# Kernel optimization log

Hardware: AMD Instinct MI355X
Metric: run time of the kernel (lower is better)

Reference implementation:

```python
import jax, jax.numpy as jnp
import numpy as np

# ---- static config ----
H, W = 60, 60
WS = 7          # window size (square)
SS = 3          # shift size
DIM = 256
NH = 8
HD = DIM // NH
N = WS * WS     # tokens per window = 49
HP = (H // WS + 1) * WS  # 63 (padded, matches __init__ mask construction)
WP = (W // WS + 1) * WS  # 63
NW = (HP // WS) * (WP // WS)  # 81 windows
EPS = 1e-5


def _rel_pos_index():
    coords = np.stack(np.meshgrid(np.arange(WS), np.arange(WS), indexing='ij'))  # (2,WS,WS)
    cf = coords.reshape(2, -1)                      # (2, N)
    rel = cf[:, :, None] - cf[:, None, :]           # (2, N, N)
    rel = rel.transpose(1, 2, 0).astype(np.int64)   # (N, N, 2)
    rel[..., 0] += WS - 1
    rel[..., 1] += WS - 1
    rel[..., 0] *= 2 * WS - 1
    return rel.sum(-1)                              # (N, N) in [0, 169)


def _attn_mask():
    img = np.zeros((HP, WP), dtype=np.float32)
    cnt = 0
    for hs in (slice(0, -WS), slice(-WS, -SS), slice(-SS, None)):
        for ws_ in (slice(0, -WS), slice(-WS, -SS), slice(-SS, None)):
            img[hs, ws_] = cnt
            cnt += 1
    mw = img.reshape(HP // WS, WS, WP // WS, WS).transpose(0, 2, 1, 3).reshape(-1, N)  # (NW, N)
    diff = mw[:, None, :] - mw[:, :, None]          # (NW, N, N)
    return np.where(diff != 0, -100.0, 0.0).astype(np.float32)


REL_IDX = _rel_pos_index()
ATTN_MASK = _attn_mask()


def layer_norm(x, g, b):
    mu = jnp.mean(x, axis=-1, keepdims=True)
    var = jnp.mean(jnp.square(x - mu), axis=-1, keepdims=True)
    return (x - mu) * jax.lax.rsqrt(var + EPS) * g + b


def setup_inputs() -> dict:
    key = jax.random.key(0)
    ks = jax.random.split(key, 8)
    B = 24
    std = 0.02
    return {
        'x': jax.random.normal(ks[0], (B, H * W, DIM), jnp.float32),
        'g1': jnp.ones((DIM,), jnp.float32),
        'b1': jnp.zeros((DIM,), jnp.float32),
        'w_qkv': jax.random.normal(ks[1], (DIM, 3 * DIM), jnp.float32) * std,
        'b_qkv': jnp.zeros((3 * DIM,), jnp.float32),
        'rel_bias_table': jax.random.normal(ks[2], ((2 * WS - 1) ** 2, NH), jnp.float32) * std,
        'w_proj': jax.random.normal(ks[3], (DIM, DIM), jnp.float32) * std,
        'b_proj': jnp.zeros((DIM,), jnp.float32),
        'g2': jnp.ones((DIM,), jnp.float32),
        'b2': jnp.zeros((DIM,), jnp.float32),
        'w_fc1': jax.random.normal(ks[4], (DIM, 4 * DIM), jnp.float32) * std,
        'b_fc1': jnp.zeros((4 * DIM,), jnp.float32),
        'w_fc2': jax.random.normal(ks[5], (4 * DIM, DIM), jnp.float32) * std,
        'b_fc2': jnp.zeros((DIM,), jnp.float32),
    }


def _swin_block(x, g1, b1, w_qkv, b_qkv, rel_bias_table, w_proj, b_proj,
                g2, b2, w_fc1, b_fc1, w_fc2, b_fc2):
    B, L, C = x.shape
    shortcut = x
    x = layer_norm(x, g1, b1).reshape(B, H, W, C)
    # pad to (HP, WP)
    x = jnp.pad(x, ((0, 0), (0, HP - H), (0, WP - W), (0, 0)))
    # cyclic shift
    x = jnp.roll(x, (-SS, -SS), axis=(1, 2))
    # window partition -> (B*NW, N, C)
    xw = x.reshape(B, HP // WS, WS, WP // WS, WS, C).transpose(0, 1, 3, 2, 4, 5)
    xw = xw.reshape(B * NW, N, C)
    # attention
    qkv = (xw @ w_qkv + b_qkv).reshape(B * NW, N, 3, NH, HD).transpose(2, 0, 3, 1, 4)
    q, k, v = qkv[0], qkv[1], qkv[2]            # (B*NW, NH, N, HD)
    q = q * (HD ** -0.5)
    attn = jnp.einsum('whnd,whmd->whnm', q, k)  # (B*NW, NH, N, N)
    rel_bias = rel_bias_table[jnp.asarray(REL_IDX)]          # (N, N, NH)
    attn = attn + rel_bias.transpose(2, 0, 1)[None]
    mask = jnp.asarray(ATTN_MASK)                            # (NW, N, N)
    attn = attn.reshape(B, NW, NH, N, N) + mask[None, :, None]
    attn = jax.nn.softmax(attn.reshape(B * NW, NH, N, N), axis=-1)
    out = jnp.einsum('whnm,whmd->whnd', attn, v)             # (B*NW, NH, N, HD)
    out = out.transpose(0, 2, 1, 3).reshape(B * NW, N, C)
    out = out @ w_proj + b_proj
    # window reverse -> (B, HP, WP, C)
    out = out.reshape(B, HP // WS, WP // WS, WS, WS, C).transpose(0, 1, 3, 2, 4, 5)
    out = out.reshape(B, HP, WP, C)
    # reverse shift, unpad
    out = jnp.roll(out, (SS, SS), axis=(1, 2))[:, :H, :W, :].reshape(B, L, C)
    x = shortcut + out
    # MLP
    y = layer_norm(x, g2, b2)
    y = jax.nn.gelu(y @ w_fc1 + b_fc1, approximate=False) @ w_fc2 + b_fc2
    return x + y


def reference(x, g1, b1, w_qkv, b_qkv, rel_bias_table, w_proj, b_proj,
              g2, b2, w_fc1, b_fc1, w_fc2, b_fc2):
    return _swin_block(x, g1, b1, w_qkv, b_qkv, rel_bias_table, w_proj, b_proj,
                       g2, b2, w_fc1, b_fc1, w_fc2, b_fc2)
```

## Files before the change

kernel.cpp:

```cpp
#include <hip/hip_runtime.h>
#include <hip/hip_bf16.h>
#include <math.h>


typedef _Float16 half8 __attribute__((ext_vector_type(8)));
typedef _Float16 half4_t __attribute__((ext_vector_type(4)));
typedef float f32x4 __attribute__((ext_vector_type(4)));

#define GLDS16(gp, lp)                                                    \
  __builtin_amdgcn_global_load_lds(                                      \
      (__attribute__((address_space(1))) const void*)(gp),               \
      (__attribute__((address_space(3))) void*)(lp), 16, 0, 0)

__device__ __forceinline__ float wave_reduce_sum(float v) {
  v += __shfl_xor(v, 1);
  v += __shfl_xor(v, 2);
  v += __shfl_xor(v, 4);
  v += __shfl_xor(v, 8);
  v += __shfl_xor(v, 16);
  v += __shfl_xor(v, 32);
  return v;
}

__global__ __launch_bounds__(256) void prep_weights(
    const float* __restrict__ wqkv, const float* __restrict__ wproj,
    const float* __restrict__ wfc1, const float* __restrict__ wfc2,
    _Float16* __restrict__ oqkv, _Float16* __restrict__ oproj,
    _Float16* __restrict__ ofc1, _Float16* __restrict__ ofc2)
{
  int idx = blockIdx.x * 256 + threadIdx.x;
  if (idx < 196608) {
    int n = idx / 256, k = idx % 256;
    oqkv[idx] = (_Float16)wqkv[k * 768 + n];
  } else if (idx < 262144) {
    int i = idx - 196608; int n = i / 256, k = i % 256;
    oproj[i] = (_Float16)wproj[k * 256 + n];
  } else if (idx < 524288) {
    int i = idx - 262144; int n = i / 256, k = i % 256;
    ofc1[i] = (_Float16)wfc1[k * 1024 + n];
  } else {
    int i = idx - 524288; int n = i / 1024, k = i % 1024;
    ofc2[i] = (_Float16)wfc2[k * 256 + n];
  }
}

__global__ __launch_bounds__(256) void prep_cb(
    const float* __restrict__ rbt, _Float16* __restrict__ cbt)
{
  int idx = blockIdx.x * 256 + threadIdx.x;
  int m = idx & 63, n = (idx >> 6) & 63;
  int hc = idx >> 12; int h = hc & 7, c = hc >> 3;
  float v;
  if (n < 49 && m < 49) {
    int i1 = n / 7, j1 = n % 7, i2 = m / 7, j2 = m % 7;
    float bias = rbt[((i1 - i2 + 6) * 13 + (j1 - j2 + 6)) * 8 + h];
    int rh1 = (c & 2) ? (i1 < 4 ? 1 : 2) : 0;
    int rh2 = (c & 2) ? (i2 < 4 ? 1 : 2) : 0;
    int rw1 = (c & 1) ? (j1 < 4 ? 1 : 2) : 0;
    int rw2 = (c & 1) ? (j2 < 4 ? 1 : 2) : 0;
    v = bias + (((rh1 != rh2) || (rw1 != rw2)) ? -100.f : 0.f);
  } else {
    v = -60000.f;
  }
  cbt[idx] = (_Float16)v;
}

__global__ __launch_bounds__(256) void ln1_window_kernel(
    const float* __restrict__ x, const float* __restrict__ g,
    const float* __restrict__ bta, _Float16* __restrict__ xw,
    int row0, int rows_c)
{
  int lrow = blockIdx.x * 4 + (threadIdx.x >> 6);
  if (lrow >= rows_c) return;
  int row = row0 + lrow;
  int lane = threadIdx.x & 63;
  int bw = row / 49, n = row - bw * 49;
  int b = bw / 81, win = bw - b * 81;
  int wh = win / 9, ww = win - wh * 9;
  int i = n / 7, j = n - i * 7;
  int sh = wh * 7 + i + 3; if (sh >= 63) sh -= 63;
  int sw = ww * 7 + j + 3; if (sw >= 63) sw -= 63;
  bool valid = (sh < 60) && (sw < 60);
  float4 v = make_float4(0.f, 0.f, 0.f, 0.f);
  if (valid)
    v = reinterpret_cast<const float4*>(x + ((size_t)b * 3600 + sh * 60 + sw) * 256)[lane];
  float s = v.x + v.y + v.z + v.w;
  s = wave_reduce_sum(s);
  float mu = s * (1.f / 256.f);
  float dx = v.x - mu, dy = v.y - mu, dz = v.z - mu, dw = v.w - mu;
  float q = dx * dx + dy * dy + dz * dz + dw * dw;
  q = wave_reduce_sum(q);
  float rs = rsqrtf(q * (1.f / 256.f) + 1e-5f);
  float4 gv = reinterpret_cast<const float4*>(g)[lane];
  float4 bv = reinterpret_cast<const float4*>(bta)[lane];
  union { _Float16 h[4]; uint2 u; } pk;
  if (valid) {
    pk.h[0] = (_Float16)(dx * rs * gv.x + bv.x);
    pk.h[1] = (_Float16)(dy * rs * gv.y + bv.y);
    pk.h[2] = (_Float16)(dz * rs * gv.z + bv.z);
    pk.h[3] = (_Float16)(dw * rs * gv.w + bv.w);
  } else {
    pk.h[0] = pk.h[1] = pk.h[2] = pk.h[3] = (_Float16)0.f;
  }
  *reinterpret_cast<uint2*>(xw + (size_t)lrow * 256 + lane * 4) = pk.u;
}

__global__ __launch_bounds__(256) void ln2_kernel(
    const float* __restrict__ xin, const float* __restrict__ g,
    const float* __restrict__ bta, _Float16* __restrict__ y)
{
  int row = blockIdx.x * 4 + (threadIdx.x >> 6);
  int lane = threadIdx.x & 63;
  float4 v = reinterpret_cast<const float4*>(xin + (size_t)row * 256)[lane];
  float s = v.x + v.y + v.z + v.w;
  s = wave_reduce_sum(s);
  float mu = s * (1.f / 256.f);
  float dx = v.x - mu, dy = v.y - mu, dz = v.z - mu, dw = v.w - mu;
  float q = dx * dx + dy * dy + dz * dz + dw * dw;
  q = wave_reduce_sum(q);
  float rs = rsqrtf(q * (1.f / 256.f) + 1e-5f);
  float4 gv = reinterpret_cast<const float4*>(g)[lane];
  float4 bv = reinterpret_cast<const float4*>(bta)[lane];
  union { _Float16 h[4]; uint2 u; } pk;
  pk.h[0] = (_Float16)(dx * rs * gv.x + bv.x);
  pk.h[1] = (_Float16)(dy * rs * gv.y + bv.y);
  pk.h[2] = (_Float16)(dz * rs * gv.z + bv.z);
  pk.h[3] = (_Float16)(dw * rs * gv.w + bv.w);
  *reinterpret_cast<uint2*>(y + (size_t)row * 256 + lane * 4) = pk.u;
}

__global__ __launch_bounds__(256) void gemm_kernel(
    const _Float16* __restrict__ A, const _Float16* __restrict__ Bt,
    const float* __restrict__ bias, const float* __restrict__ resid,
    void* __restrict__ out, int M, int N, int K, int mode, int row0)
{
  __shared__ __align__(16) _Float16 As[4096];
  __shared__ __align__(16) _Float16 Bs[4096];
  const int tid = threadIdx.x;
  const int m0 = blockIdx.x * 128, n0 = blockIdx.y * 128;
  const int wv = tid >> 6, ln = tid & 63;
  const int wm = (wv >> 1) * 64, wn = (wv & 1) * 64;
  const int quad = ln >> 4, l16 = ln & 15;

  const int r0 = wv * 32 + (ln >> 2);
  const int r1 = r0 + 16;
  const int sg0 = (((ln & 3) ^ ((r0 >> 1) & 3)) << 3);
  const int sg1 = (((ln & 3) ^ ((r1 >> 1) & 3)) << 3);
  int gmA0 = m0 + r0; if (gmA0 >= M) gmA0 = M - 1;
  int gmA1 = m0 + r1; if (gmA1 >= M) gmA1 = M - 1;
  const _Float16* pA0 = A + (size_t)gmA0 * K + sg0;
  const _Float16* pA1 = A + (size_t)gmA1 * K + sg1;
  const _Float16* pB0 = Bt + (size_t)(n0 + r0) * K + sg0;
  const _Float16* pB1 = Bt + (size_t)(n0 + r1) * K + sg1;
  _Float16* ldsA0 = As + wv * 1024;
  _Float16* ldsA1 = As + wv * 1024 + 512;
  _Float16* ldsB0 = Bs + wv * 1024;
  _Float16* ldsB1 = Bs + wv * 1024 + 512;

  const half8* pa[4]; const half8* pb[4];
#pragma unroll
  for (int i = 0; i < 4; i++) {
    int ra = wm + i * 16 + l16;
    pa[i] = reinterpret_cast<const half8*>(&As[ra * 32 + ((quad ^ ((ra >> 1) & 3)) << 3)]);
    int rb = wn + i * 16 + l16;
    pb[i] = reinterpret_cast<const half8*>(&Bs[rb * 32 + ((quad ^ ((rb >> 1) & 3)) << 3)]);
  }

  f32x4 acc[4][4];
#pragma unroll
  for (int i = 0; i < 4; i++)
#pragma unroll
    for (int j = 0; j < 4; j++) acc[i][j] = (f32x4)0.f;

  for (int k0 = 0; k0 < K; k0 += 32) {
    GLDS16(pA0 + k0, ldsA0);
    GLDS16(pA1 + k0, ldsA1);
    GLDS16(pB0 + k0, ldsB0);
    GLDS16(pB1 + k0, ldsB1);
    __syncthreads();
    half8 af[4], bf[4];
#pragma unroll
    for (int i = 0; i < 4; i++) { af[i] = *pa[i]; bf[i] = *pb[i]; }
#pragma unroll
    for (int i = 0; i < 4; i++)
#pragma unroll
      for (int j = 0; j < 4; j++)
        acc[i][j] = __builtin_amdgcn_mfma_f32_16x16x32_f16(af[i], bf[j], acc[i][j], 0, 0, 0);
    __syncthreads();
  }

  float bq[4];
#pragma unroll
  for (int j = 0; j < 4; j++) bq[j] = bias[n0 + wn + j * 16 + l16];

#pragma unroll
  for (int i = 0; i < 4; i++) {
#pragma unroll
    for (int r = 0; r < 4; r++) {
      int gm = m0 + wm + i * 16 + quad * 4 + r;
      if (gm >= M) continue;
      if (mode == 0) {
        _Float16* op = reinterpret_cast<_Float16*>(out) + (size_t)gm * N;
#pragma unroll
        for (int j = 0; j < 4; j++) {
          int gn = n0 + wn + j * 16 + l16;
          float v = acc[i][j][r] + bq[j];
          if (gn < 256) v *= 0.17677669529663687f;
          op[gn] = (_Float16)v;
        }
      } else if (mode == 2) {
        _Float16* op = reinterpret_cast<_Float16*>(out) + (size_t)gm * N;
#pragma unroll
        for (int j = 0; j < 4; j++) {
          int gn = n0 + wn + j * 16 + l16;
          float v = acc[i][j][r] + bq[j];
          v = 0.5f * v * (1.f + erff(v * 0.70710678118654752f));
          op[gn] = (_Float16)v;
        }
      } else if (mode == 3) {
        float* op = reinterpret_cast<float*>(out) + (size_t)gm * N;
        const float* rp = resid + (size_t)gm * N;
#pragma unroll
        for (int j = 0; j < 4; j++) {
          int gn = n0 + wn + j * 16 + l16;
          op[gn] = rp[gn] + acc[i][j][r] + bq[j];
        }
      } else {
        int gmg = gm + row0;
        int bw = gmg / 49, nn = gmg - bw * 49;
        int bb = bw / 81, win = bw - bb * 81;
        int wh = win / 9, wwn = win - wh * 9;
        int ii = nn / 7, jj = nn - ii * 7;
        int sh = wh * 7 + ii + 3; if (sh >= 63) sh -= 63;
        int sw = wwn * 7 + jj + 3; if (sw >= 63) sw -= 63;
        if (sh < 60 && sw < 60) {
          size_t o = ((size_t)bb * 3600 + sh * 60 + sw) * 256;
          float* op = reinterpret_cast<float*>(out) + o;
          const float* rp = resid + o;
#pragma unroll
          for (int j = 0; j < 4; j++) {
            int gn = n0 + wn + j * 16 + l16;
            op[gn] = rp[gn] + acc[i][j][r] + bq[j];
          }
        }
      }
    }
  }
}

__global__ __launch_bounds__(64) void attn_mfma(
    const _Float16* __restrict__ qkv, const _Float16* __restrict__ cbt,
    _Float16* __restrict__ outp)
{
  __shared__ __align__(16) _Float16 VT[32][72];
  __shared__ __align__(16) _Float16 Ps[64][72];
  const int bwh = blockIdx.x;
  const int bw = bwh >> 3, h = bwh & 7;
  const int win = bw % 81;
  const int wh = win / 9, ww = win - wh * 9;
  const int cls = ((wh == 8) ? 2 : 0) | ((ww == 8) ? 1 : 0);
  const int lane = threadIdx.x;
  const int quad = lane >> 4, l16 = lane & 15;

  for (int e = lane; e < 480; e += 64) {
    int d = e / 15, m = 49 + e % 15;
    VT[d][m] = (_Float16)0.f;
  }
  const size_t vbase = (size_t)bw * 49 * 768 + 512 + h * 32;
  for (int e = lane; e < 1568; e += 64) {
    int m = e >> 5, d = e & 31;
    VT[d][m] = qkv[vbase + (size_t)m * 768 + d];
  }

  const _Float16* qb = qkv + (size_t)bw * 49 * 768 + h * 32 + quad * 8;
  half8 kf[4], qf[4];
  const half8 hz = (half8)(_Float16)0.f;
#pragma unroll
  for (int t = 0; t < 4; t++) {
    int row = t * 16 + l16;
    int rc = row < 49 ? row : 48;
    half8 kv = *reinterpret_cast<const half8*>(qb + 256 + (size_t)rc * 768);
    half8 qv = *reinterpret_cast<const half8*>(qb + (size_t)rc * 768);
    kf[t] = row < 49 ? kv : hz;
    qf[t] = row < 49 ? qv : hz;
  }

  f32x4 S[4][4];
#pragma unroll
  for (int mt = 0; mt < 4; mt++)
#pragma unroll
    for (int nt = 0; nt < 4; nt++) S[mt][nt] = (f32x4)0.f;
#pragma unroll
  for (int mt = 0; mt < 4; mt++)
#pragma unroll
    for (int nt = 0; nt < 4; nt++)
      S[mt][nt] = __builtin_amdgcn_mfma_f32_16x16x32_f16(kf[mt], qf[nt], S[mt][nt], 0, 0, 0);

  const _Float16* cbp = cbt + (((size_t)cls * 8 + h) << 12);
#pragma unroll
  for (int nt = 0; nt < 4; nt++) {
    int n = nt * 16 + l16;
#pragma unroll
    for (int mt = 0; mt < 4; mt++) {
      half4_t cb4 = *reinterpret_cast<const half4_t*>(cbp + n * 64 + mt * 16 + quad * 4);
#pragma unroll
      for (int r = 0; r < 4; r++) S[mt][nt][r] += (float)cb4[r];
    }
  }

  float inv[4];
#pragma unroll
  for (int nt = 0; nt < 4; nt++) {
    float mx = -3.0e38f;
#pragma unroll
    for (int mt = 0; mt < 4; mt++)
#pragma unroll
      for (int r = 0; r < 4; r++) mx = fmaxf(mx, S[mt][nt][r]);
    mx = fmaxf(mx, __shfl_xor(mx, 16));
    mx = fmaxf(mx, __shfl_xor(mx, 32));
    float sm = 0.f;
#pragma unroll
    for (int mt = 0; mt < 4; mt++)
#pragma unroll
      for (int r = 0; r < 4; r++) {
        float e = __expf(S[mt][nt][r] - mx);
        S[mt][nt][r] = e;
        sm += e;
      }
    sm += __shfl_xor(sm, 16);
    sm += __shfl_xor(sm, 32);
    inv[nt] = 1.f / sm;
  }

#pragma unroll
  for (int nt = 0; nt < 4; nt++) {
#pragma unroll
    for (int mt = 0; mt < 4; mt++) {
      half4_t p;
#pragma unroll
      for (int r = 0; r < 4; r++) p[r] = (_Float16)(S[mt][nt][r] * inv[nt]);
      *reinterpret_cast<half4_t*>(&Ps[nt * 16 + l16][mt * 16 + quad * 4]) = p;
    }
  }
  __syncthreads();

  f32x4 O[2][4];
#pragma unroll
  for (int dt = 0; dt < 2; dt++)
#pragma unroll
    for (int nt = 0; nt < 4; nt++) O[dt][nt] = (f32x4)0.f;
#pragma unroll
  for (int ks = 0; ks < 2; ks++) {
    half8 va[2], pb[4];
#pragma unroll
    for (int dt = 0; dt < 2; dt++)
      va[dt] = *reinterpret_cast<const half8*>(&VT[dt * 16 + l16][ks * 32 + quad * 8]);
#pragma unroll
    for (int nt = 0; nt < 4; nt++)
      pb[nt] = *reinterpret_cast<const half8*>(&Ps[nt * 16 + l16][ks * 32 + quad * 8]);
#pragma unroll
    for (int dt = 0; dt < 2; dt++)
#pragma unroll
      for (int nt = 0; nt < 4; nt++)
        O[dt][nt] = __builtin_amdgcn_mfma_f32_16x16x32_f16(va[dt], pb[nt], O[dt][nt], 0, 0, 0);
  }

#pragma unroll
  for (int nt = 0; nt < 4; nt++) {
    int n = nt * 16 + l16;
    if (n < 49) {
#pragma unroll
      for (int dt = 0; dt < 2; dt++) {
        half4_t o4;
#pragma unroll
        for (int r = 0; r < 4; r++) o4[r] = (_Float16)O[dt][nt][r];
        *reinterpret_cast<half4_t*>(
            outp + ((size_t)bw * 49 + n) * 256 + h * 32 + dt * 16 + quad * 4) = o4;
      }
    }
  }
}

extern "C" void kernel_launch(void* const* d_in, const int* in_sizes, int n_in,
                              void* d_out, int out_size, void* d_ws, size_t ws_size,
                              hipStream_t stream) {
  const float* x      = (const float*)d_in[0];
  const float* g1     = (const float*)d_in[1];
  const float* b1     = (const float*)d_in[2];
  const float* w_qkv  = (const float*)d_in[3];
  const float* b_qkv  = (const float*)d_in[4];
  const float* rbt    = (const float*)d_in[5];
  const float* w_proj = (const float*)d_in[6];
  const float* b_proj = (const float*)d_in[7];
  const float* g2     = (const float*)d_in[8];
  const float* b2     = (const float*)d_in[9];
  const float* w_fc1  = (const float*)d_in[10];
  const float* b_fc1  = (const float*)d_in[11];
  const float* w_fc2  = (const float*)d_in[12];
  const float* b_fc2  = (const float*)d_in[13];
  float* outp = (float*)d_out;

  char* ws = (char*)d_ws;
  _Float16* wqkvT  = (_Float16*)(ws + 0);
  _Float16* wprojT = (_Float16*)(ws + 393216);
  _Float16* wfc1T  = (_Float16*)(ws + 524288);
  _Float16* wfc2T  = (_Float16*)(ws + 1048576);
  _Float16* cbt    = (_Float16*)(ws + 1572864);
  const size_t WB = 1835008;

  const int cand[8] = {24, 12, 8, 6, 4, 3, 2, 1};
  int cb = 1;
  for (int ci = 0; ci < 8; ci++) {
    size_t need = WB + (size_t)cand[ci] * (2032128u + 7372800u);
    if (ws_size >= need) { cb = cand[ci]; break; }
  }
  const int nch = 24 / cb;

  _Float16* r1 = (_Float16*)(ws + WB);
  _Float16* r2 = (_Float16*)(ws + WB + (size_t)cb * 2032128u);

  prep_weights<<<3072, 256, 0, stream>>>(w_qkv, w_proj, w_fc1, w_fc2,
                                         wqkvT, wprojT, wfc1T, wfc2T);
  prep_cb<<<512, 256, 0, stream>>>(rbt, cbt);

  for (int c = 0; c < nch; c++) {
    const int b0 = c * cb;
    const int rows_att = cb * 81 * 49;
    const int row0_att = b0 * 81 * 49;
    const int rows_mlp = cb * 3600;
    const int row0_mlp = b0 * 3600;

    ln1_window_kernel<<<(rows_att + 3) / 4, 256, 0, stream>>>(
        x, g1, b1, r1, row0_att, rows_att);
    {
      dim3 g((rows_att + 127) / 128, 6);
      gemm_kernel<<<g, 256, 0, stream>>>(r1, wqkvT, b_qkv, nullptr, r2,
                                         rows_att, 768, 256, 0, 0);
    }
    attn_mfma<<<cb * 81 * 8, 64, 0, stream>>>(r2, cbt, r1);
    {
      dim3 g((rows_att + 127) / 128, 2);
      gemm_kernel<<<g, 256, 0, stream>>>(r1, wprojT, b_proj, x, outp,
                                         rows_att, 256, 256, 1, row0_att);
    }
    ln2_kernel<<<rows_mlp / 4, 256, 0, stream>>>(
        outp + (size_t)row0_mlp * 256, g2, b2, r1);
    {
      dim3 g((rows_mlp + 127) / 128, 8);
      gemm_kernel<<<g, 256, 0, stream>>>(r1, wfc1T, b_fc1, nullptr, r2,
                                         rows_mlp, 1024, 256, 2, 0);
    }
    {
      dim3 g((rows_mlp + 127) / 128, 2);
      float* od = outp + (size_t)row0_mlp * 256;
      gemm_kernel<<<g, 256, 0, stream>>>(r2, wfc2T, b_fc2, od, od,
                                         rows_mlp, 256, 1024, 3, 0);
    }
  }
}
```

Baseline: 648.8 us.

## Double-buffer GEMM LDS with BK=64, swap grid order, vectorize epilogue stores

The GEMM now loads 64-wide K tiles into a double-buffered LDS area, so the next tile is fetched while MFMAs run on the current one. It also uses a new XOR swizzle and cuts the K-loop barriers from two per 32-wide step to one per 64-wide step. The MFMA operands are swapped so each lane holds four consecutive columns of one output row, which allows vector half4 and float4 stores and vector bias loads. The grid axes are swapped so N tiles vary fastest, for better reuse of A rows in cache. LDS use grows to 64 KB per block with a launch-bounds occupancy hint of 2, which may limit blocks per CU.

```diff
diff --git a/kernel.cpp b/kernel.cpp
--- a/kernel.cpp
+++ b/kernel.cpp
@@ -129,41 +129,40 @@
   *reinterpret_cast<uint2*>(y + (size_t)row * 256 + lane * 4) = pk.u;
 }
 
-__global__ __launch_bounds__(256) void gemm_kernel(
+__global__ __launch_bounds__(256, 2) void gemm_kernel(
     const _Float16* __restrict__ A, const _Float16* __restrict__ Bt,
     const float* __restrict__ bias, const float* __restrict__ resid,
     void* __restrict__ out, int M, int N, int K, int mode, int row0)
 {
-  __shared__ __align__(16) _Float16 As[4096];
-  __shared__ __align__(16) _Float16 Bs[4096];
+  __shared__ __align__(16) _Float16 lds[2][2][8192];
   const int tid = threadIdx.x;
-  const int m0 = blockIdx.x * 128, n0 = blockIdx.y * 128;
+  const int n0 = blockIdx.x * 128, m0 = blockIdx.y * 128;
   const int wv = tid >> 6, ln = tid & 63;
   const int wm = (wv >> 1) * 64, wn = (wv & 1) * 64;
   const int quad = ln >> 4, l16 = ln & 15;
 
-  const int r0 = wv * 32 + (ln >> 2);
-  const int r1 = r0 + 16;
-  const int sg0 = (((ln & 3) ^ ((r0 >> 1) & 3)) << 3);
-  const int sg1 = (((ln & 3) ^ ((r1 >> 1) & 3)) << 3);
-  int gmA0 = m0 + r0; if (gmA0 >= M) gmA0 = M - 1;
-  int gmA1 = m0 + r1; if (gmA1 >= M) gmA1 = M - 1;
-  const _Float16* pA0 = A + (size_t)gmA0 * K + sg0;
-  const _Float16* pA1 = A + (size_t)gmA1 * K + sg1;
-  const _Float16* pB0 = Bt + (size_t)(n0 + r0) * K + sg0;
-  const _Float16* pB1 = Bt + (size_t)(n0 + r1) * K + sg1;
-  _Float16* ldsA0 = As + wv * 1024;
-  _Float16* ldsA1 = As + wv * 1024 + 512;
-  _Float16* ldsB0 = Bs + wv * 1024;
-  _Float16* ldsB1 = Bs + wv * 1024 + 512;
-
-  const half8* pa[4]; const half8* pb[4];
+  const int rl = ln >> 3;
+  const int gseg = ((ln & 7) ^ rl) << 3;
+  const _Float16* gA[4]; const _Float16* gB[4];
+#pragma unroll
+  for (int s = 0; s < 4; s++) {
+    int r = wv * 32 + s * 8 + rl;
+    int gm = m0 + r; if (gm >= M) gm = M - 1;
+    gA[s] = A + (size_t)gm * K + gseg;
+    gB[s] = Bt + (size_t)(n0 + r) * K + gseg;
+  }
+
+  int offA[2][4], offB[2][4];
 #pragma unroll
   for (int i = 0; i < 4; i++) {
     int ra = wm + i * 16 + l16;
-    pa[i] = reinterpret_cast<const half8*>(&As[ra * 32 + ((quad ^ ((ra >> 1) & 3)) << 3)]);
     int rb = wn + i * 16 + l16;
-    pb[i] = reinterpret_cast<const half8*>(&Bs[rb * 32 + ((quad ^ ((rb >> 1) & 3)) << 3)]);
+    int sw0 = l16 & 7;
+#pragma unroll
+    for (int ks = 0; ks < 2; ks++) {
+      offA[ks][i] = ra * 64 + (((ks * 4 + quad) ^ sw0) << 3);
+      offB[ks][i] = rb * 64 + (((ks * 4 + quad) ^ sw0) << 3);
+    }
   }
 
   f32x4 acc[4][4];
@@ -172,76 +171,103 @@
 #pragma unroll
     for (int j = 0; j < 4; j++) acc[i][j] = (f32x4)0.f;
 
-  for (int k0 = 0; k0 < K; k0 += 32) {
-    GLDS16(pA0 + k0, ldsA0);
-    GLDS16(pA1 + k0, ldsA1);
-    GLDS16(pB0 + k0, ldsB0);
-    GLDS16(pB1 + k0, ldsB1);
+#define STAGE(buf, koff)                                                   \
+  {                                                                        \
+    _Float16* la = &lds[buf][0][wv * 2048];                                \
+    _Float16* lb = &lds[buf][1][wv * 2048];                                \
+    GLDS16(gA[0] + (koff), la);        GLDS16(gB[0] + (koff), lb);         \
+    GLDS16(gA[1] + (koff), la + 512);  GLDS16(gB[1] + (koff), lb + 512);   \
+    GLDS16(gA[2] + (koff), la + 1024); GLDS16(gB[2] + (koff), lb + 1024);  \
+    GLDS16(gA[3] + (koff), la + 1536); GLDS16(gB[3] + (koff), lb + 1536);  \
+  }
+
+  const int nt = K >> 6;
+  STAGE(0, 0);
+  __syncthreads();
+  for (int t = 0; t < nt; t++) {
+    const int cur = t & 1;
+    half8 a0[4], b0[4], a1[4], b1[4];
+#pragma unroll
+    for (int i = 0; i < 4; i++) {
+      a0[i] = *reinterpret_cast<const half8*>(&lds[cur][0][offA[0][i]]);
+      a1[i] = *reinterpret_cast<const half8*>(&lds[cur][0][offA[1][i]]);
+      b0[i] = *reinterpret_cast<const half8*>(&lds[cur][1][offB[0][i]]);
+      b1[i] = *reinterpret_cast<const half8*>(&lds[cur][1][offB[1][i]]);
+    }
+    if (t + 1 < nt) STAGE(cur ^ 1, (t + 1) << 6);
+#pragma unroll
+    for (int i = 0; i < 4; i++)
+#pragma unroll
+      for (int j = 0; j < 4; j++)
+        acc[i][j] = __builtin_amdgcn_mfma_f32_16x16x32_f16(b0[j], a0[i], acc[i][j], 0, 0, 0);
+#pragma unroll
+    for (int i = 0; i < 4; i++)
+#pragma unroll
+      for (int j = 0; j < 4; j++)
+        acc[i][j] = __builtin_amdgcn_mfma_f32_16x16x32_f16(b1[j], a1[i], acc[i][j], 0, 0, 0);
     __syncthreads();
-    half8 af[4], bf[4];
-#pragma unroll
-    for (int i = 0; i < 4; i++) { af[i] = *pa[i]; bf[i] = *pb[i]; }
-#pragma unroll
-    for (int i = 0; i < 4; i++)
-#pragma unroll
-      for (int j = 0; j < 4; j++)
-        acc[i][j] = __builtin_amdgcn_mfma_f32_16x16x32_f16(af[i], bf[j], acc[i][j], 0, 0, 0);
-    __syncthreads();
-  }
-
-  float bq[4];
-#pragma unroll
-  for (int j = 0; j < 4; j++) bq[j] = bias[n0 + wn + j * 16 + l16];
+  }
+#undef STAGE
+
+  f32x4 bias4[4];
+#pragma unroll
+  for (int j = 0; j < 4; j++)
+    bias4[j] = *reinterpret_cast<const f32x4*>(bias + n0 + wn + j * 16 + quad * 4);
 
 #pragma unroll
   for (int i = 0; i < 4; i++) {
-#pragma unroll
-    for (int r = 0; r < 4; r++) {
-      int gm = m0 + wm + i * 16 + quad * 4 + r;
-      if (gm >= M) continue;
-      if (mode == 0) {
-        _Float16* op = reinterpret_cast<_Float16*>(out) + (size_t)gm * N;
+    int gm = m0 + wm + i * 16 + l16;
+    if (gm >= M) continue;
+    if (mode == 0) {
+      _Float16* op = reinterpret_cast<_Float16*>(out) + (size_t)gm * N + n0 + wn;
+#pragma unroll
+      for (int j = 0; j < 4; j++) {
+        float sc = (n0 + wn + j * 16) < 256 ? 0.17677669529663687f : 1.f;
+        half4_t o4;
+#pragma unroll
+        for (int r = 0; r < 4; r++)
+          o4[r] = (_Float16)((acc[i][j][r] + bias4[j][r]) * sc);
+        *reinterpret_cast<half4_t*>(op + j * 16 + quad * 4) = o4;
+      }
+    } else if (mode == 2) {
+      _Float16* op = reinterpret_cast<_Float16*>(out) + (size_t)gm * N + n0 + wn;
+#pragma unroll
+      for (int j = 0; j < 4; j++) {
+        half4_t o4;
+#pragma unroll
+        for (int r = 0; r < 4; r++) {
+          float v = acc[i][j][r] + bias4[j][r];
+          v = 0.5f * v * (1.f + erff(v * 0.70710678118654752f));
+          o4[r] = (_Float16)v;
+        }
+        *reinterpret_cast<half4_t*>(op + j * 16 + quad * 4) = o4;
+      }
+    } else if (mode == 3) {
+      float* op = reinterpret_cast<float*>(out) + (size_t)gm * N + n0 + wn;
+      const float* rp = resid + (size_t)gm * N + n0 + wn;
+#pragma unroll
+      for (int j = 0; j < 4; j++) {
+        f32x4 rv = *reinterpret_cast<const f32x4*>(rp + j * 16 + quad * 4);
+        f32x4 v = acc[i][j] + bias4[j] + rv;
+        *reinterpret_cast<f32x4*>(op + j * 16 + quad * 4) = v;
+      }
+    } else {
+      int gmg = gm + row0;
+      int bw = gmg / 49, nn = gmg - bw * 49;
+      int bidx = bw / 81, win = bw - bidx * 81;
+      int wh = win / 9, wwn = win - wh * 9;
+      int ii = nn / 7, jj = nn - ii * 7;
+      int sh = wh * 7 + ii + 3; if (sh >= 63) sh -= 63;
+      int sw = wwn * 7 + jj + 3; if (sw >= 63) sw -= 63;
+      if (sh < 60 && sw < 60) {
+        size_t o = ((size_t)bidx * 3600 + sh * 60 + sw) * 256 + n0 + wn;
+        float* op = reinterpret_cast<float*>(out) + o;
+        const float* rp = resid + o;
 #pragma unroll
         for (int j = 0; j < 4; j++) {
-          int gn = n0 + wn + j * 16 + l16;
-          float v = acc[i][j][r] + bq[j];
-          if (gn < 256) v *= 0.17677669529663687f;
-          op[gn] = (_Float16)v;
-        }
-      } else if (mode == 2) {
-        _Float16* op = reinterpret_cast<_Float16*>(out) + (size_t)gm * N;
-#pragma unroll
-        for (int j = 0; j < 4; j++) {
-          int gn = n0 + wn + j * 16 + l16;
-          float v = acc[i][j][r] + bq[j];
-          v = 0.5f * v * (1.f + erff(v * 0.70710678118654752f));
-          op[gn] = (_Float16)v;
-        }
-      } else if (mode == 3) {
-        float* op = reinterpret_cast<float*>(out) + (size_t)gm * N;
-        const float* rp = resid + (size_t)gm * N;
-#pragma unroll
-        for (int j = 0; j < 4; j++) {
-          int gn = n0 + wn + j * 16 + l16;
-          op[gn] = rp[gn] + acc[i][j][r] + bq[j];
-        }
-      } else {
-        int gmg = gm + row0;
-        int bw = gmg / 49, nn = gmg - bw * 49;
-        int bb = bw / 81, win = bw - bb * 81;
-        int wh = win / 9, wwn = win - wh * 9;
-        int ii = nn / 7, jj = nn - ii * 7;
-        int sh = wh * 7 + ii + 3; if (sh >= 63) sh -= 63;
-        int sw = wwn * 7 + jj + 3; if (sw >= 63) sw -= 63;
-        if (sh < 60 && sw < 60) {
-          size_t o = ((size_t)bb * 3600 + sh * 60 + sw) * 256;
-          float* op = reinterpret_cast<float*>(out) + o;
-          const float* rp = resid + o;
-#pragma unroll
-          for (int j = 0; j < 4; j++) {
-            int gn = n0 + wn + j * 16 + l16;
-            op[gn] = rp[gn] + acc[i][j][r] + bq[j];
-          }
+          f32x4 rv = *reinterpret_cast<const f32x4*>(rp + j * 16 + quad * 4);
+          f32x4 v = acc[i][j] + bias4[j] + rv;
+          *reinterpret_cast<f32x4*>(op + j * 16 + quad * 4) = v;
         }
       }
     }
@@ -433,25 +459,25 @@
     ln1_window_kernel<<<(rows_att + 3) / 4, 256, 0, stream>>>(
         x, g1, b1, r1, row0_att, rows_att);
     {
-      dim3 g((rows_att + 127) / 128, 6);
+      dim3 g(6, (rows_att + 127) / 128);
       gemm_kernel<<<g, 256, 0, stream>>>(r1, wqkvT, b_qkv, nullptr, r2,
                                          rows_att, 768, 256, 0, 0);
     }
     attn_mfma<<<cb * 81 * 8, 64, 0, stream>>>(r2, cbt, r1);
     {
-      dim3 g((rows_att + 127) / 128, 2);
+      dim3 g(2, (rows_att + 127) / 128);
       gemm_kernel<<<g, 256, 0, stream>>>(r1, wprojT, b_proj, x, outp,
                                          rows_att, 256, 256, 1, row0_att);
     }
     ln2_kernel<<<rows_mlp / 4, 256, 0, stream>>>(
         outp + (size_t)row0_mlp * 256, g2, b2, r1);
     {
-      dim3 g((rows_mlp + 127) / 128, 8);
+      dim3 g(8, (rows_mlp + 127) / 128);
       gemm_kernel<<<g, 256, 0, stream>>>(r1, wfc1T, b_fc1, nullptr, r2,
                                          rows_mlp, 1024, 256, 2, 0);
     }
     {
-      dim3 g((rows_mlp + 127) / 128, 2);
+      dim3 g(2, (rows_mlp + 127) / 128);
       float* od = outp + (size_t)row0_mlp * 256;
       gemm_kernel<<<g, 256, 0, stream>>>(r2, wfc2T, b_fc2, od, od,
                                          rows_mlp, 256, 1024, 3, 0);
```

Result: faster. 626.1 us (-3.5%).
